# Performance work log

Measured on AMD Instinct MI355X. Metric: run time of the kernel, lower is better.

Reference implementation:

```python
import jax, jax.numpy as jnp
import numpy as np
from jax import lax

NEG_SLOPE = 0.2
BN_EPS = 1e-5


def _edges(n_nodes, n_total):
    # complete graph (no self loops) on the first n_nodes nodes, as in create_complete_graph,
    # plus PyG GATConv default add_self_loops over ALL n_total nodes.
    i = np.arange(n_nodes)
    src = np.repeat(i, n_nodes)
    dst = np.tile(i, n_nodes)
    keep = src != dst
    loops = np.arange(n_total)
    src = np.concatenate([src[keep], loops]).astype(np.int32)
    dst = np.concatenate([dst[keep], loops]).astype(np.int32)
    return jnp.asarray(src), jnp.asarray(dst)


def _bn_eval(x, g, b, m, v):
    # x: [B, C, H, W]; eval-mode batchnorm with running stats
    inv = g / jnp.sqrt(v + BN_EPS)
    return x * inv[None, :, None, None] + (b - m * inv)[None, :, None, None]


def _gat(x, W, a_src, a_dst, bias, src, dst, n_total):
    h = x @ W                      # [N, D_out]
    s = h @ a_src                  # [N] per-node source score
    d = h @ a_dst                  # [N] per-node dest score
    e = jax.nn.leaky_relu(s[src] + d[dst], NEG_SLOPE)          # [E]
    emax = jax.ops.segment_max(e, dst, num_segments=n_total)   # [N]
    ex = jnp.exp(e - emax[dst])
    denom = jax.ops.segment_sum(ex, dst, num_segments=n_total)
    alpha = ex / denom[dst]                                    # [E]
    out = jax.ops.segment_sum(alpha[:, None] * h[src], dst, num_segments=n_total)
    return out + bias


def setup_inputs() -> dict:
    key = jax.random.key(0)
    ks = jax.random.split(key, 12)
    B, H, W = 8, 64, 64

    def rn(k, shape, s):
        return jax.random.normal(k, shape, jnp.float32) * s

    return {
        "images": jax.random.normal(ks[0], (B, 3, H, W), jnp.float32),
        "conv1_w": rn(ks[1], (64, 3, 3, 3), 0.1), "conv1_b": jnp.zeros((64,), jnp.float32),
        "bn1_g": jnp.ones((64,), jnp.float32), "bn1_b": jnp.zeros((64,), jnp.float32),
        "bn1_m": jnp.zeros((64,), jnp.float32), "bn1_v": jnp.ones((64,), jnp.float32),
        "conv2_w": rn(ks[2], (128, 64, 3, 3), 0.05), "conv2_b": jnp.zeros((128,), jnp.float32),
        "bn2_g": jnp.ones((128,), jnp.float32), "bn2_b": jnp.zeros((128,), jnp.float32),
        "bn2_m": jnp.zeros((128,), jnp.float32), "bn2_v": jnp.ones((128,), jnp.float32),
        "gat1_w": rn(ks[3], (128, 256), 0.05), "gat1_asrc": rn(ks[4], (256,), 0.05),
        "gat1_adst": rn(ks[5], (256,), 0.05), "gat1_bias": jnp.zeros((256,), jnp.float32),
        "gat2_w": rn(ks[6], (256, 128), 0.05), "gat2_asrc": rn(ks[7], (128,), 0.05),
        "gat2_adst": rn(ks[8], (128,), 0.05), "gat2_bias": jnp.zeros((128,), jnp.float32),
        "out_w": rn(ks[9], (128, 10), 0.05), "out_b": jnp.zeros((10,), jnp.float32),
    }


def reference(images, conv1_w, conv1_b, bn1_g, bn1_b, bn1_m, bn1_v,
              conv2_w, conv2_b, bn2_g, bn2_b, bn2_m, bn2_v,
              gat1_w, gat1_asrc, gat1_adst, gat1_bias,
              gat2_w, gat2_asrc, gat2_adst, gat2_bias,
              out_w, out_b):
    dn = ("NCHW", "OIHW", "NCHW")
    x = lax.conv_general_dilated(images, conv1_w, (1, 1), "SAME", dimension_numbers=dn)
    x = x + conv1_b[None, :, None, None]
    x = jax.nn.relu(_bn_eval(x, bn1_g, bn1_b, bn1_m, bn1_v))
    x = lax.reduce_window(x, -jnp.inf, lax.max, (1, 1, 2, 2), (1, 1, 2, 2), "VALID")
    x = lax.conv_general_dilated(x, conv2_w, (1, 1), "SAME", dimension_numbers=dn)
    x = x + conv2_b[None, :, None, None]
    x = jax.nn.relu(_bn_eval(x, bn2_g, bn2_b, bn2_m, bn2_v))

    B = x.shape[0]
    n_nodes = x.shape[2] * x.shape[3]          # (H/2)*(W/2) = 1024
    x = x.reshape(B, 128, n_nodes).transpose(0, 2, 1).reshape(-1, 128)  # [B*n, 128]
    n_total = B * n_nodes
    src, dst = _edges(n_nodes, n_total)

    x = jax.nn.relu(_gat(x, gat1_w, gat1_asrc, gat1_adst, gat1_bias, src, dst, n_total))
    x = jax.nn.relu(_gat(x, gat2_w, gat2_asrc, gat2_adst, gat2_bias, src, dst, n_total))

    x = x.reshape(B, n_nodes, 128).mean(axis=1)   # global_mean_pool over each image's nodes
    logits = x @ out_w + out_b
    return jax.nn.log_softmax(logits, axis=1)
```

## Files before the change

### kernel.cpp

```cpp
#include <hip/hip_runtime.h>
#include <math.h>

#define BN_EPS 1e-5f
#define NEG_SLOPE 0.2f

__device__ __forceinline__ float relu_f(float x) { return x > 0.f ? x : 0.f; }
__device__ __forceinline__ float leaky_f(float z) { return z > 0.f ? z : NEG_SLOPE * z; }

__global__ void conv1_pool(const float* __restrict__ img, const float* __restrict__ w,
                           const float* __restrict__ cb, const float* __restrict__ g,
                           const float* __restrict__ bb, const float* __restrict__ m,
                           const float* __restrict__ vv, float* __restrict__ out)
{
    int blk = blockIdx.x;
    int q = blk & 3, cog = (blk >> 2) & 15, b = blk >> 6;
    int t = threadIdx.x;
    int x = t & 31, y = (q << 3) + (t >> 5);

    float acc[4][4] = {};
#pragma unroll
    for (int ci = 0; ci < 3; ++ci) {
        const float* ib = img + (b * 3 + ci) * 4096;
        float rv[4][4];
#pragma unroll
        for (int r = 0; r < 4; ++r) {
            int yy = 2 * y - 1 + r;
            bool yok = (unsigned)yy < 64u;
            const float* p = ib + yy * 64 + 2 * x;
            float2 c01 = yok ? *(const float2*)p : make_float2(0.f, 0.f);
            rv[r][1] = c01.x;
            rv[r][2] = c01.y;
            rv[r][0] = (yok && x > 0) ? p[-1] : 0.f;
            rv[r][3] = (yok && x < 31) ? p[2] : 0.f;
        }
#pragma unroll
        for (int j = 0; j < 4; ++j) {
            const float* wj = w + ((cog * 4 + j) * 3 + ci) * 9;
#pragma unroll
            for (int ky = 0; ky < 3; ++ky)
#pragma unroll
                for (int kx = 0; kx < 3; ++kx) {
                    float wvv = wj[ky * 3 + kx];
#pragma unroll
                    for (int py = 0; py < 2; ++py)
#pragma unroll
                        for (int px = 0; px < 2; ++px)
                            acc[j][py * 2 + px] += rv[py + ky][px + kx] * wvv;
                }
        }
    }
#pragma unroll
    for (int j = 0; j < 4; ++j) {
        int co = cog * 4 + j;
        float inv = g[co] / sqrtf(vv[co] + BN_EPS);
        float sh = cb[co] * inv + (bb[co] - m[co] * inv);
        float v0 = relu_f(acc[j][0] * inv + sh);
        float v1 = relu_f(acc[j][1] * inv + sh);
        float v2 = relu_f(acc[j][2] * inv + sh);
        float v3 = relu_f(acc[j][3] * inv + sh);
        out[((b * 64 + co) * 32 + y) * 32 + x] = fmaxf(fmaxf(v0, v1), fmaxf(v2, v3));
    }
}

__global__ void conv2_fused(const float* __restrict__ in, const float* __restrict__ w,
                            const float* __restrict__ cb, const float* __restrict__ g,
                            const float* __restrict__ bb, const float* __restrict__ m,
                            const float* __restrict__ vv, float* __restrict__ x0)
{
    int blk = blockIdx.x;
    int half = blk & 1, cog = (blk >> 1) & 31, b = blk >> 6;
    int t = threadIdx.x;
    int x2p = (t & 15) * 2;
    int y = half * 16 + (t >> 4);
    bool xnz = x2p != 0;
    bool xhi = x2p == 30;
    const float* ibase = in + b * 64 * 1024;
    int xb = xnz ? x2p - 1 : 0;

    float acc[4][2] = {};

#pragma unroll 2
    for (int ci = 0; ci < 64; ++ci) {
        const float* cb2 = ibase + ci * 1024;
        float rc[3][4];
#pragma unroll
        for (int r = 0; r < 3; ++r) {
            int yy = y - 1 + r;
            bool yok = (unsigned)yy < 32u;
            const float* p = cb2 + yy * 32 + xb;
            float4 f = yok ? *(const float4*)p : make_float4(0.f, 0.f, 0.f, 0.f);
            rc[r][0] = xnz ? f.x : 0.f;
            rc[r][1] = xnz ? f.y : f.x;
            rc[r][2] = xnz ? f.z : f.y;
            float r3 = xnz ? f.w : f.z;
            rc[r][3] = xhi ? 0.f : r3;
        }
#pragma unroll
        for (int j = 0; j < 4; ++j) {
            const float* wj = w + ((cog * 4 + j) * 64 + ci) * 9;
#pragma unroll
            for (int ky = 0; ky < 3; ++ky)
#pragma unroll
                for (int kx = 0; kx < 3; ++kx) {
                    float wvv = wj[ky * 3 + kx];
                    acc[j][0] += rc[ky][kx] * wvv;
                    acc[j][1] += rc[ky][kx + 1] * wvv;
                }
        }
    }

    float o0[4], o1[4];
#pragma unroll
    for (int j = 0; j < 4; ++j) {
        int co = cog * 4 + j;
        float inv = g[co] / sqrtf(vv[co] + BN_EPS);
        float sh = cb[co] * inv + (bb[co] - m[co] * inv);
        o0[j] = relu_f(acc[j][0] * inv + sh);
        o1[j] = relu_f(acc[j][1] * inv + sh);
    }
    int n0 = b * 1024 + y * 32 + x2p;
    float4 s0 = {o0[0], o0[1], o0[2], o0[3]};
    float4 s1 = {o1[0], o1[1], o1[2], o1[3]};
    *(float4*)&x0[(size_t)n0 * 128 + cog * 4] = s0;
    *(float4*)&x0[(size_t)(n0 + 1) * 128 + cog * 4] = s1;
}

template <int K, int N>
__global__ void gemm32(const float* __restrict__ A, const float* __restrict__ B,
                       float* __restrict__ C)
{
    __shared__ float As[16][32];
    __shared__ float Bs[16][64];
    int t = threadIdx.x;
    int m0 = blockIdx.x * 32;
    int n0 = blockIdx.y * 64;
    int tx = t & 15, ty = t >> 4;
    int am = t >> 2, akq = (t & 3) * 4;
    float acc[4][4] = {};

    for (int k0 = 0; k0 < K; k0 += 16) {
        float4 av = *(const float4*)&A[(size_t)(m0 + am) * K + k0 + akq];
        float4 bv0 = *(const float4*)&B[(size_t)(k0 + ty) * N + n0 + tx * 4];
        float4 bv1 = *(const float4*)&B[(size_t)(k0 + 8 + ty) * N + n0 + tx * 4];
        __syncthreads();
        As[akq + 0][am] = av.x;
        As[akq + 1][am] = av.y;
        As[akq + 2][am] = av.z;
        As[akq + 3][am] = av.w;
        *(float4*)&Bs[ty][tx * 4] = bv0;
        *(float4*)&Bs[ty + 8][tx * 4] = bv1;
        __syncthreads();
#pragma unroll
        for (int kk = 0; kk < 16; ++kk) {
            float4 a4 = *(const float4*)&As[kk][ty * 4];
            float4 b4 = *(const float4*)&Bs[kk][tx * 4];
            float aa[4] = {a4.x, a4.y, a4.z, a4.w};
            float bb4[4] = {b4.x, b4.y, b4.z, b4.w};
#pragma unroll
            for (int i = 0; i < 4; ++i)
#pragma unroll
                for (int j = 0; j < 4; ++j)
                    acc[i][j] += aa[i] * bb4[j];
        }
    }
#pragma unroll
    for (int i = 0; i < 4; ++i) {
        float4 o = {acc[i][0], acc[i][1], acc[i][2], acc[i][3]};
        *(float4*)&C[(size_t)(m0 + ty * 4 + i) * N + n0 + tx * 4] = o;
    }
}

__global__ void score_kernel(const float* __restrict__ h, const float* __restrict__ asrc,
                             const float* __restrict__ adst, float* __restrict__ s,
                             float* __restrict__ d, int D, int N)
{
    int gt = blockIdx.x * blockDim.x + threadIdx.x;
    int wave = gt >> 6, lane = gt & 63;
    if (wave >= N) return;
    const float* hp = h + (size_t)wave * D;
    float ss = 0.f, dd = 0.f;
    for (int c = lane; c < D; c += 64) {
        float hv = hp[c];
        ss += hv * asrc[c];
        dd += hv * adst[c];
    }
    for (int off = 32; off; off >>= 1) {
        ss += __shfl_down(ss, off);
        dd += __shfl_down(dd, off);
    }
    if (lane == 0) { s[wave] = ss; d[wave] = dd; }
}

template <int D, int KS>
__global__ void gat_agg_gemm(const float* __restrict__ h, const float* __restrict__ s,
                             const float* __restrict__ d, float* __restrict__ pacc,
                             float* __restrict__ pden)
{
    __shared__ float Ss[1024];
    __shared__ float As[16][32];
    __shared__ float Bs[16][64];
    __shared__ float red[2];
    __shared__ float part[16][32];

    const int CH = 1024 / KS;
    int t = threadIdx.x;
    int m0 = blockIdx.x * 32;
    int n0 = blockIdx.y * 64;
    int kz = blockIdx.z;
    int tx = t & 15, ty = t >> 4;
    int ug = t >> 3, vg4 = (t & 7) * 4;

    float4 sa = *(const float4*)&s[t * 8];
    float4 sb = *(const float4*)&s[t * 8 + 4];
    *(float4*)&Ss[t * 8] = sa;
    *(float4*)&Ss[t * 8 + 4] = sb;
    float lm = fmaxf(fmaxf(fmaxf(sa.x, sa.y), fmaxf(sa.z, sa.w)),
                     fmaxf(fmaxf(sb.x, sb.y), fmaxf(sb.z, sb.w)));
#pragma unroll
    for (int off = 1; off < 64; off <<= 1) lm = fmaxf(lm, __shfl_xor(lm, off));
    if ((t & 63) == 0) red[t >> 6] = lm;
    __syncthreads();
    float smax = fmaxf(red[0], red[1]);

    float4 dv = *(const float4*)&d[m0 + vg4];
    float4 mv = {leaky_f(smax + dv.x), leaky_f(smax + dv.y),
                 leaky_f(smax + dv.z), leaky_f(smax + dv.w)};
    float4 dsum = {0.f, 0.f, 0.f, 0.f};
    float acc[4][4] = {};

    for (int k0 = kz * CH; k0 < kz * CH + CH; k0 += 16) {
        float4 bv0 = *(const float4*)&h[(size_t)(k0 + ty) * D + n0 + tx * 4];
        float4 bv1 = *(const float4*)&h[(size_t)(k0 + 8 + ty) * D + n0 + tx * 4];
        float su = Ss[k0 + ug];
        float4 avv;
        avv.x = __expf(leaky_f(su + dv.x) - mv.x);
        avv.y = __expf(leaky_f(su + dv.y) - mv.y);
        avv.z = __expf(leaky_f(su + dv.z) - mv.z);
        avv.w = __expf(leaky_f(su + dv.w) - mv.w);
        dsum.x += avv.x; dsum.y += avv.y; dsum.z += avv.z; dsum.w += avv.w;
        __syncthreads();
        *(float4*)&As[ug][vg4] = avv;
        *(float4*)&Bs[ty][tx * 4] = bv0;
        *(float4*)&Bs[ty + 8][tx * 4] = bv1;
        __syncthreads();
#pragma unroll
        for (int kk = 0; kk < 16; ++kk) {
            float4 a4 = *(const float4*)&As[kk][ty * 4];
            float4 b4 = *(const float4*)&Bs[kk][tx * 4];
            float aa[4] = {a4.x, a4.y, a4.z, a4.w};
            float bb4[4] = {b4.x, b4.y, b4.z, b4.w};
#pragma unroll
            for (int i = 0; i < 4; ++i)
#pragma unroll
                for (int j = 0; j < 4; ++j)
                    acc[i][j] += aa[i] * bb4[j];
        }
    }

    __syncthreads();
    *(float4*)&part[ug][vg4] = dsum;
    __syncthreads();

#pragma unroll
    for (int i = 0; i < 4; ++i) {
        int r = ty * 4 + i;
        float4 o = {acc[i][0], acc[i][1], acc[i][2], acc[i][3]};
        *(float4*)&pacc[((size_t)kz * 1024 + m0 + r) * D + n0 + tx * 4] = o;
    }
    if (t < 32) {
        float den = 0.f;
#pragma unroll
        for (int u = 0; u < 16; ++u) den += part[u][t];
        pden[kz * 1024 + m0 + t] = den;
    }
}

template <int D, int KS>
__global__ void gat_combine(const float* __restrict__ pacc, const float* __restrict__ pden,
                            const float* __restrict__ bias, float* __restrict__ out)
{
    int idx = blockIdx.x * blockDim.x + threadIdx.x;
    if (idx >= 1024 * D / 4) return;
    int c4 = idx & (D / 4 - 1);
    int v = idx / (D / 4);
    float4 a = {0.f, 0.f, 0.f, 0.f};
    float den = 0.f;
#pragma unroll
    for (int ks = 0; ks < KS; ++ks) {
        float4 p = ((const float4*)pacc)[(size_t)(ks * 1024 + v) * (D / 4) + c4];
        a.x += p.x; a.y += p.y; a.z += p.z; a.w += p.w;
        den += pden[ks * 1024 + v];
    }
    float rd = 1.f / den;
    float4 bz = ((const float4*)bias)[c4];
    float4 o = {relu_f(a.x * rd + bz.x), relu_f(a.y * rd + bz.y),
                relu_f(a.z * rd + bz.z), relu_f(a.w * rd + bz.w)};
    ((float4*)out)[(size_t)v * (D / 4) + c4] = o;
}

template <int D>
__global__ void gat_self4(const float* __restrict__ h, const float* __restrict__ bias,
                          float* __restrict__ out)
{
    int idx = blockIdx.x * blockDim.x + threadIdx.x;
    if (idx >= 7168 * D / 4) return;
    int c4 = idx & (D / 4 - 1);
    int n = 1024 + idx / (D / 4);
    float4 v = ((const float4*)h)[(size_t)n * (D / 4) + c4];
    float4 bz = ((const float4*)bias)[c4];
    float4 o = {relu_f(v.x + bz.x), relu_f(v.y + bz.y),
                relu_f(v.z + bz.z), relu_f(v.w + bz.w)};
    ((float4*)out)[(size_t)n * (D / 4) + c4] = o;
}

__global__ void pool_part(const float* __restrict__ x2, float* __restrict__ part)
{
    int b = blockIdx.x >> 4, seg = blockIdx.x & 15, t = threadIdx.x;
    const float* p = x2 + ((size_t)b * 1024 + seg * 64) * 128 + t;
    float acc = 0.f;
#pragma unroll 8
    for (int n = 0; n < 64; ++n) acc += p[(size_t)n * 128];
    part[(b * 16 + seg) * 128 + t] = acc;
}

__global__ void head_kernel(const float* __restrict__ part, const float* __restrict__ ow,
                            const float* __restrict__ ob, float* __restrict__ out)
{
    __shared__ float pooled[128];
    __shared__ float logits[10];
    int b = blockIdx.x, t = threadIdx.x;
    float acc = 0.f;
#pragma unroll
    for (int sgi = 0; sgi < 16; ++sgi) acc += part[(b * 16 + sgi) * 128 + t];
    pooled[t] = acc * (1.f / 1024.f);
    __syncthreads();
    if (t < 10) {
        float l = ob[t];
        for (int c = 0; c < 128; ++c) l += pooled[c] * ow[c * 10 + t];
        logits[t] = l;
    }
    __syncthreads();
    if (t == 0) {
        float mx = logits[0];
        for (int j = 1; j < 10; ++j) mx = fmaxf(mx, logits[j]);
        float sum = 0.f;
        for (int j = 0; j < 10; ++j) sum += expf(logits[j] - mx);
        float lse = mx + logf(sum);
        for (int j = 0; j < 10; ++j) out[b * 10 + j] = logits[j] - lse;
    }
}

extern "C" void kernel_launch(void* const* d_in, const int* in_sizes, int n_in,
                              void* d_out, int out_size, void* d_ws, size_t ws_size,
                              hipStream_t stream)
{
    const float* images = (const float*)d_in[0];
    const float* c1w = (const float*)d_in[1];
    const float* c1b = (const float*)d_in[2];
    const float* bn1g = (const float*)d_in[3];
    const float* bn1b = (const float*)d_in[4];
    const float* bn1m = (const float*)d_in[5];
    const float* bn1v = (const float*)d_in[6];
    const float* c2w = (const float*)d_in[7];
    const float* c2b = (const float*)d_in[8];
    const float* bn2g = (const float*)d_in[9];
    const float* bn2b = (const float*)d_in[10];
    const float* bn2m = (const float*)d_in[11];
    const float* bn2v = (const float*)d_in[12];
    const float* g1w = (const float*)d_in[13];
    const float* g1as = (const float*)d_in[14];
    const float* g1ad = (const float*)d_in[15];
    const float* g1b = (const float*)d_in[16];
    const float* g2w = (const float*)d_in[17];
    const float* g2as = (const float*)d_in[18];
    const float* g2ad = (const float*)d_in[19];
    const float* g2b = (const float*)d_in[20];
    const float* ow = (const float*)d_in[21];
    const float* ob = (const float*)d_in[22];
    float* out = (float*)d_out;

    float* ws = (float*)d_ws;
    float* x1    = ws;
    float* bufc1 = ws + 2097152;
    float* h1    = ws + 2621440;
    float* x0    = ws + 4718592;
    float* h2    = ws + 5767168;
    float* s1    = ws + 6815744;
    float* d1    = ws + 6816768;
    float* s2    = ws + 6817792;
    float* d2    = ws + 6818816;
    float* part  = bufc1;
    float* pden1 = bufc1 + 16384;
    float* pden2 = bufc1 + 24576;
    float* pacc1 = x0;
    float* pacc2 = h1;
    float* x2    = x0;

    conv1_pool<<<512, 256, 0, stream>>>(images, c1w, c1b, bn1g, bn1b, bn1m, bn1v, bufc1);
    conv2_fused<<<512, 256, 0, stream>>>(bufc1, c2w, c2b, bn2g, bn2b, bn2m, bn2v, x0);

    gemm32<128, 256><<<dim3(256, 4), 128, 0, stream>>>(x0, g1w, h1);
    score_kernel<<<256, 256, 0, stream>>>(h1, g1as, g1ad, s1, d1, 256, 1024);
    gat_agg_gemm<256, 8><<<dim3(32, 4, 8), 128, 0, stream>>>(h1, s1, d1, pacc1, pden1);
    gat_combine<256, 8><<<256, 256, 0, stream>>>(pacc1, pden1, g1b, x1);
    gat_self4<256><<<1792, 256, 0, stream>>>(h1, g1b, x1);

    gemm32<256, 128><<<dim3(256, 2), 128, 0, stream>>>(x1, g2w, h2);
    score_kernel<<<256, 256, 0, stream>>>(h2, g2as, g2ad, s2, d2, 128, 1024);
    gat_agg_gemm<128, 16><<<dim3(32, 2, 16), 128, 0, stream>>>(h2, s2, d2, pacc2, pden2);
    gat_combine<128, 16><<<128, 256, 0, stream>>>(pacc2, pden2, g2b, x2);
    gat_self4<128><<<896, 256, 0, stream>>>(h2, g2b, x2);

    pool_part<<<128, 128, 0, stream>>>(x2, part);
    head_kernel<<<8, 128, 0, stream>>>(part, ow, ob, out);
}
```

Before: 217.3 us.

## Split conv2 input-channel reduction four ways with a separate combine kernel

```diff
diff --git a/kernel.cpp b/kernel.cpp
--- a/kernel.cpp
+++ b/kernel.cpp
@@ -62,25 +62,23 @@
     }
 }
 
-__global__ void conv2_fused(const float* __restrict__ in, const float* __restrict__ w,
-                            const float* __restrict__ cb, const float* __restrict__ g,
-                            const float* __restrict__ bb, const float* __restrict__ m,
-                            const float* __restrict__ vv, float* __restrict__ x0)
+__global__ void conv2_split(const float* __restrict__ in, const float* __restrict__ w,
+                            float* __restrict__ pacc01, float* __restrict__ pacc23)
 {
     int blk = blockIdx.x;
-    int half = blk & 1, cog = (blk >> 1) & 31, b = blk >> 6;
+    int kz = blk & 3, half = (blk >> 2) & 1, cog = (blk >> 3) & 31, b = blk >> 8;
     int t = threadIdx.x;
     int x2p = (t & 15) * 2;
     int y = half * 16 + (t >> 4);
     bool xnz = x2p != 0;
     bool xhi = x2p == 30;
-    const float* ibase = in + b * 64 * 1024;
+    const float* ibase = in + b * 64 * 1024 + kz * 16 * 1024;
     int xb = xnz ? x2p - 1 : 0;
 
     float acc[4][2] = {};
 
 #pragma unroll 2
-    for (int ci = 0; ci < 64; ++ci) {
+    for (int ci = 0; ci < 16; ++ci) {
         const float* cb2 = ibase + ci * 1024;
         float rc[3][4];
 #pragma unroll
@@ -97,7 +95,7 @@
         }
 #pragma unroll
         for (int j = 0; j < 4; ++j) {
-            const float* wj = w + ((cog * 4 + j) * 64 + ci) * 9;
+            const float* wj = w + ((cog * 4 + j) * 64 + kz * 16 + ci) * 9;
 #pragma unroll
             for (int ky = 0; ky < 3; ++ky)
 #pragma unroll
@@ -109,20 +107,49 @@
         }
     }
 
-    float o0[4], o1[4];
-#pragma unroll
-    for (int j = 0; j < 4; ++j) {
-        int co = cog * 4 + j;
-        float inv = g[co] / sqrtf(vv[co] + BN_EPS);
-        float sh = cb[co] * inv + (bb[co] - m[co] * inv);
-        o0[j] = relu_f(acc[j][0] * inv + sh);
-        o1[j] = relu_f(acc[j][1] * inv + sh);
-    }
     int n0 = b * 1024 + y * 32 + x2p;
-    float4 s0 = {o0[0], o0[1], o0[2], o0[3]};
-    float4 s1 = {o1[0], o1[1], o1[2], o1[3]};
-    *(float4*)&x0[(size_t)n0 * 128 + cog * 4] = s0;
-    *(float4*)&x0[(size_t)(n0 + 1) * 128 + cog * 4] = s1;
+    float* pp = (kz & 2 ? pacc23 : pacc01) + (size_t)(kz & 1) * 1048576;
+    float4 s0 = {acc[0][0], acc[1][0], acc[2][0], acc[3][0]};
+    float4 s1 = {acc[0][1], acc[1][1], acc[2][1], acc[3][1]};
+    *(float4*)&pp[(size_t)n0 * 128 + cog * 4] = s0;
+    *(float4*)&pp[(size_t)(n0 + 1) * 128 + cog * 4] = s1;
+}
+
+__global__ void conv2_combine(const float* __restrict__ pacc01, const float* __restrict__ pacc23,
+                              const float* __restrict__ cb, const float* __restrict__ g,
+                              const float* __restrict__ bb, const float* __restrict__ m,
+                              const float* __restrict__ vv, float* __restrict__ x0)
+{
+    int idx = blockIdx.x * blockDim.x + threadIdx.x;
+    int c4 = idx & 31;
+    const float4* p01 = (const float4*)pacc01;
+    const float4* p23 = (const float4*)pacc23;
+    float4 a0 = p01[idx];
+    float4 a1 = p01[idx + 262144];
+    float4 a2 = p23[idx];
+    float4 a3 = p23[idx + 262144];
+    float sx = a0.x + a1.x + a2.x + a3.x;
+    float sy = a0.y + a1.y + a2.y + a3.y;
+    float sz = a0.z + a1.z + a2.z + a3.z;
+    float sw = a0.w + a1.w + a2.w + a3.w;
+
+    float4 gg = ((const float4*)g)[c4];
+    float4 vvv = ((const float4*)vv)[c4];
+    float4 bbb = ((const float4*)bb)[c4];
+    float4 mm = ((const float4*)m)[c4];
+    float4 cbb = ((const float4*)cb)[c4];
+    float ix = gg.x / sqrtf(vvv.x + BN_EPS);
+    float iy = gg.y / sqrtf(vvv.y + BN_EPS);
+    float iz = gg.z / sqrtf(vvv.z + BN_EPS);
+    float iw = gg.w / sqrtf(vvv.w + BN_EPS);
+    float shx = cbb.x * ix + (bbb.x - mm.x * ix);
+    float shy = cbb.y * iy + (bbb.y - mm.y * iy);
+    float shz = cbb.z * iz + (bbb.z - mm.z * iz);
+    float shw = cbb.w * iw + (bbb.w - mm.w * iw);
+
+    float4 o = {relu_f(sx * ix + shx), relu_f(sy * iy + shy),
+                relu_f(sz * iz + shz), relu_f(sw * iw + shw)};
+    ((float4*)x0)[idx] = o;
 }
 
 template <int K, int N>
@@ -395,9 +422,12 @@
     float* pacc1 = x0;
     float* pacc2 = h1;
     float* x2    = x0;
+    float* c2p01 = x1;
+    float* c2p23 = h1;
 
     conv1_pool<<<512, 256, 0, stream>>>(images, c1w, c1b, bn1g, bn1b, bn1m, bn1v, bufc1);
-    conv2_fused<<<512, 256, 0, stream>>>(bufc1, c2w, c2b, bn2g, bn2b, bn2m, bn2v, x0);
+    conv2_split<<<2048, 256, 0, stream>>>(bufc1, c2w, c2p01, c2p23);
+    conv2_combine<<<1024, 256, 0, stream>>>(c2p01, c2p23, c2b, bn2g, bn2b, bn2m, bn2v, x0);
 
     gemm32<128, 256><<<dim3(256, 4), 128, 0, stream>>>(x0, g1w, h1);
     score_kernel<<<256, 256, 0, stream>>>(h1, g1as, g1ad, s1, d1, 256, 1024);
```

Result: no change. 215.2 us (-0.9%).
